# Optimization experiments

Measured on AMD Instinct MI355X. Metric: run time of the kernel, lower is better.

## Reference

```python
import jax, jax.numpy as jnp
import numpy as np

N_NODES = 50000
N_EDGES = 1_600_000
D_IN, D_HID, D_OUT = 128, 512, 64


def _graph_conv(h, src, dst, W_rel, b_rel, W_root, n_nodes):
    # PyG GraphConv with aggr='add':
    #   out_i = W_rel @ (sum_{j->i} h_j) + b_rel + W_root @ h_i
    agg = jax.ops.segment_sum(h[src], dst, num_segments=n_nodes)  # [N, d]
    return agg @ W_rel + b_rel + h @ W_root


def setup_inputs() -> dict:
    key = jax.random.key(0)
    ks = jax.random.split(key, 12)
    def glorot(k, shape):
        fan_in, fan_out = shape
        lim = (6.0 / (fan_in + fan_out)) ** 0.5
        return jax.random.uniform(k, shape, jnp.float32, -lim, lim)
    x = jax.random.normal(ks[0], (N_NODES, D_IN), jnp.float32)
    edge_index = jax.random.randint(ks[1], (2, N_EDGES), 0, N_NODES, jnp.int64)
    return {
        "x": x,
        "W1_rel": glorot(ks[2], (D_IN, D_HID)),
        "b1": jnp.zeros((D_HID,), jnp.float32),
        "W1_root": glorot(ks[3], (D_IN, D_HID)),
        "W2_rel": glorot(ks[4], (D_HID, D_HID)),
        "b2": jnp.zeros((D_HID,), jnp.float32),
        "W2_root": glorot(ks[5], (D_HID, D_HID)),
        "W3_rel": glorot(ks[6], (D_HID, D_HID)),
        "b3": jnp.zeros((D_HID,), jnp.float32),
        "W3_root": glorot(ks[7], (D_HID, D_HID)),
        "W_lin": glorot(ks[8], (D_HID, D_OUT)),
        "b_lin": jnp.zeros((D_OUT,), jnp.float32),
        "edge_index": edge_index,
    }


def reference(x, W1_rel, b1, W1_root, W2_rel, b2, W2_root,
              W3_rel, b3, W3_root, W_lin, b_lin, edge_index):
    n = x.shape[0]
    src, dst = edge_index[0], edge_index[1]
    h = jax.nn.relu(_graph_conv(x, src, dst, W1_rel, b1, W1_root, n))
    h = jax.nn.relu(_graph_conv(h, src, dst, W2_rel, b2, W2_root, n))
    h = jax.nn.relu(_graph_conv(h, src, dst, W3_rel, b3, W3_root, n))
    node_embed = h
    # dropout is identity in eval mode; final linear head
    logits = h @ W_lin + b_lin
    return (logits, node_embed)
```

## Files before the change

### kernel.cpp

```cpp
#include <hip/hip_runtime.h>


typedef unsigned short u16;
typedef unsigned int u32;
typedef unsigned char u8;

#define NN 50000
#define NE 1600000
#define MPAD 50176
#define GRID_M ((NN + 127) / 128)
#define NBKT 98
#define CAP 20480
#define STG 18432

using frag8 = __attribute__((ext_vector_type(8))) short;
using f32x4 = __attribute__((ext_vector_type(4))) float;
using f32x2 = __attribute__((ext_vector_type(2))) float;

__device__ __forceinline__ u16 f2bf(float f) {
  u32 u = __float_as_uint(f);
  u32 r = u + 0x7fffu + ((u >> 16) & 1u);
  return (u16)(r >> 16);
}
__device__ __forceinline__ float lo2f(u32 u) { return __uint_as_float(u << 16); }
__device__ __forceinline__ float hi2f(u32 u) { return __uint_as_float(u & 0xffff0000u); }
__device__ __forceinline__ u32 pack2(float a, float b) {
  return (u32)f2bf(a) | ((u32)f2bf(b) << 16);
}

__device__ __forceinline__ void g2l16(const void* g, void* l) {
  __builtin_amdgcn_global_load_lds((const __attribute__((address_space(1))) void*)g,
                                   (__attribute__((address_space(3))) void*)l, 16, 0, 0);
}

__device__ __forceinline__ int swz(int s) { return s ^ ((s >> 3) & 3); }


__global__ void zero_i32(int* p, int n) {
  int i = blockIdx.x * 256 + threadIdx.x;
  if (i < n) p[i] = 0;
}

__global__ __launch_bounds__(256) void p1bin(const int* __restrict__ src,
                                             const int* __restrict__ dst,
                                             int* __restrict__ gcur,
                                             u32* __restrict__ region, int ne) {
  __shared__ u32 lbuf[NBKT * 64];
  __shared__ int lcnt[NBKT];
  __shared__ int gbase[NBKT];
  const int tid = threadIdx.x;
  if (tid < NBKT) lcnt[tid] = 0;
  __syncthreads();
  const int base = blockIdx.x * 2048;
#pragma unroll
  for (int j = 0; j < 8; ++j) {
    int i = base + j * 256 + tid;
    if (i < ne) {
      int d = dst[i];
      int s = src[i];
      int b = d >> 9;
      u32 entry = ((u32)(d & 511) << 16) | (u32)s;
      int slot = atomicAdd(&lcnt[b], 1);
      if (slot < 64) lbuf[b * 64 + slot] = entry;
      else {
        int g = atomicAdd(&gcur[b], 1);
        region[(size_t)b * CAP + g] = entry;
      }
    }
  }
  __syncthreads();
  if (tid < NBKT) {
    int c = min(lcnt[tid], 64);
    gbase[tid] = atomicAdd(&gcur[tid], c);
  }
  __syncthreads();
  const int wv = tid >> 6, lane = tid & 63;
  for (int b = wv; b < NBKT; b += 4) {
    int c = min(lcnt[b], 64);
    int gb = gbase[b];
    for (int s2 = lane; s2 < c; s2 += 64)
      region[(size_t)b * CAP + gb + s2] = lbuf[b * 64 + s2];
  }
}

__global__ void scan98(const int* __restrict__ gcur, int* __restrict__ bbase,
                       int* __restrict__ rs) {
  if (threadIdx.x == 0) {
    int run = 0;
    for (int b = 0; b < NBKT; ++b) {
      bbase[b] = run;
      run += gcur[b];
    }
    bbase[NBKT] = run;
    rs[NN] = run;
  }
}

__global__ __launch_bounds__(256) void p2build(const u32* __restrict__ region,
                                               const int* __restrict__ gcnt,
                                               const int* __restrict__ bbase,
                                               int* __restrict__ rs,
                                               u16* __restrict__ csr) {
  __shared__ int cnt[512];
  __shared__ int off[512];
  __shared__ int sh[256];
  __shared__ u16 stg[STG];
  const int b = blockIdx.x, tid = threadIdx.x;
  const int n0 = b * 512;
  const int nnb = min(512, NN - n0);
  const int ec = gcnt[b];
  const int gb = bbase[b];
  const u32* __restrict__ reg = region + (size_t)b * CAP;
  cnt[tid] = 0;
  cnt[tid + 256] = 0;
  __syncthreads();
  for (int i = tid; i < ec; i += 256) atomicAdd(&cnt[reg[i] >> 16], 1);
  __syncthreads();
  int c0 = cnt[2 * tid], c1 = cnt[2 * tid + 1];
  int s = c0 + c1;
  sh[tid] = s;
  __syncthreads();
  for (int o = 1; o < 256; o <<= 1) {
    int t2 = (tid >= o) ? sh[tid - o] : 0;
    __syncthreads();
    sh[tid] += t2;
    __syncthreads();
  }
  int base0 = sh[tid] - s;
  off[2 * tid] = base0;
  off[2 * tid + 1] = base0 + c0;
  __syncthreads();
  if (2 * tid < nnb) rs[n0 + 2 * tid] = gb + off[2 * tid];
  if (2 * tid + 1 < nnb) rs[n0 + 2 * tid + 1] = gb + off[2 * tid + 1];
  cnt[2 * tid] = off[2 * tid];
  cnt[2 * tid + 1] = off[2 * tid + 1];
  __syncthreads();
  for (int i = tid; i < ec; i += 256) {
    u32 e = reg[i];
    int slot = atomicAdd(&cnt[e >> 16], 1);
    u16 sv = (u16)(e & 0xffff);
    if (slot < STG) stg[slot] = sv;
    else csr[gb + slot] = sv;
  }
  __syncthreads();
  for (int i = tid; i < ec && i < STG; i += 256) csr[gb + i] = stg[i];
}


__global__ void f2bf_x(const float4* __restrict__ in, u16* __restrict__ out, int n4) {
  int i = blockIdx.x * 256 + threadIdx.x;
  if (i < n4) {
    float4 v = in[i];
    int node = i >> 5;
    int w = i & 31;
    uint2 o;
    o.x = pack2(v.x, v.y);
    o.y = pack2(v.z, v.w);
    *(uint2*)(out + (size_t)node * 256 + 128 + w * 4) = o;
  }
}

__global__ void wtrans(const float* __restrict__ Wa, int Ka, const float* __restrict__ Wb,
                       int Kb, int N, u16* __restrict__ out) {
  int idx = blockIdx.x * 256 + threadIdx.x;
  int Kt = Ka + Kb;
  if (idx >= N * Kt) return;
  int n = idx / Kt;
  int k = idx - n * Kt;
  float v = (k < Ka) ? Wa[(size_t)k * N + n] : Wb[(size_t)(k - Ka) * N + n];
  out[idx] = f2bf(v);
}


__device__ __forceinline__ void accb(f32x2* a, uint4 v, float s) {
  f32x2 sv = (f32x2){s, s};
  f32x2 f;
  f.x = lo2f(v.x); f.y = hi2f(v.x); a[0] += f * sv;
  f.x = lo2f(v.y); f.y = hi2f(v.y); a[1] += f * sv;
  f.x = lo2f(v.z); f.y = hi2f(v.z); a[2] += f * sv;
  f.x = lo2f(v.w); f.y = hi2f(v.w); a[3] += f * sv;
}

__global__ __launch_bounds__(256) void agg_bf128(const u16* __restrict__ H, int ldh,
                                                 u16* __restrict__ Out, int ldo,
                                                 const int* __restrict__ rs,
                                                 const u16* __restrict__ csr, int n) {
  int w = (blockIdx.x * 256 + threadIdx.x) >> 6;
  int lane = threadIdx.x & 63;
  if (w >= n) return;
  int beg = rs[w], end = rs[w + 1];
  const int q = lane >> 4;
  const int lsub = lane & 15;
  f32x2 acc[4];
#pragma unroll
  for (int i = 0; i < 4; ++i) acc[i] = (f32x2){0.f, 0.f};

  int e = beg;
  for (; e + 16 <= end; e += 16) {
    int si[4];
#pragma unroll
    for (int u = 0; u < 4; ++u) si[u] = csr[e + 4 * u + q];
    uint4 v[4];
#pragma unroll
    for (int u = 0; u < 4; ++u)
      v[u] = *(const uint4*)(H + (size_t)si[u] * ldh + lsub * 8);
#pragma unroll
    for (int u = 0; u < 4; ++u) accb(acc, v[u], 1.f);
  }
  if (e < end) {
#pragma unroll
    for (int u = 0; u < 4; ++u) {
      int ei = e + 4 * u + q;
      int ec = min(ei, end - 1);
      int s0 = csr[ec];
      uint4 v = *(const uint4*)(H + (size_t)s0 * ldh + lsub * 8);
      accb(acc, v, (ei < end) ? 1.f : 0.f);
    }
  }
#pragma unroll
  for (int i = 0; i < 4; ++i) {
    acc[i].x += __shfl_xor(acc[i].x, 16);
    acc[i].y += __shfl_xor(acc[i].y, 16);
    acc[i].x += __shfl_xor(acc[i].x, 32);
    acc[i].y += __shfl_xor(acc[i].y, 32);
  }
  if (lane < 32) {
    int qq = lane >> 4;
    uint2 o;
    o.x = pack2(acc[qq * 2].x, acc[qq * 2].y);
    o.y = pack2(acc[qq * 2 + 1].x, acc[qq * 2 + 1].y);
    *(uint2*)(Out + (size_t)w * ldo + (lane & 15) * 8 + qq * 4) = o;
  }
}


__device__ __forceinline__ void accp(f32x2* a, uint4 v, float s) {
  f32x2 sv = (f32x2){s, s};
  f32x2 f;
  f = __builtin_amdgcn_cvt_pk_f32_fp8(v.x, false); a[0] += f * sv;
  f = __builtin_amdgcn_cvt_pk_f32_fp8(v.x, true);  a[1] += f * sv;
  f = __builtin_amdgcn_cvt_pk_f32_fp8(v.y, false); a[2] += f * sv;
  f = __builtin_amdgcn_cvt_pk_f32_fp8(v.y, true);  a[3] += f * sv;
  f = __builtin_amdgcn_cvt_pk_f32_fp8(v.z, false); a[4] += f * sv;
  f = __builtin_amdgcn_cvt_pk_f32_fp8(v.z, true);  a[5] += f * sv;
  f = __builtin_amdgcn_cvt_pk_f32_fp8(v.w, false); a[6] += f * sv;
  f = __builtin_amdgcn_cvt_pk_f32_fp8(v.w, true);  a[7] += f * sv;
}

__global__ __launch_bounds__(256) void agg_fp8(const u8* __restrict__ H8,
                                               const float* __restrict__ sc,
                                               u16* __restrict__ Out,
                                               const int* __restrict__ rs,
                                               const u16* __restrict__ csr, int n) {
  int w = (blockIdx.x * 256 + threadIdx.x) >> 6;
  int lane = threadIdx.x & 63;
  if (w >= n) return;
  int beg = rs[w], end = rs[w + 1];
  const int halfe = lane >> 5;
  const int lsub = lane & 31;
  const int shalf = lsub >> 4;
  f32x2 acc[8];
#pragma unroll
  for (int i = 0; i < 8; ++i) acc[i] = (f32x2){0.f, 0.f};

  int e = beg;
  for (; e + 8 <= end; e += 8) {
    int si[4];
#pragma unroll
    for (int u = 0; u < 4; ++u) si[u] = csr[e + 2 * u + halfe];
    uint4 v[4];
#pragma unroll
    for (int u = 0; u < 4; ++u)
      v[u] = *(const uint4*)(H8 + (size_t)si[u] * 512 + lsub * 16);
    float cs[4];
#pragma unroll
    for (int u = 0; u < 4; ++u) cs[u] = sc[si[u] * 2 + shalf];
#pragma unroll
    for (int u = 0; u < 4; ++u) accp(acc, v[u], cs[u]);
  }
  if (e < end) {
#pragma unroll
    for (int u = 0; u < 4; ++u) {
      int ei = e + 2 * u + halfe;
      int ec = min(ei, end - 1);
      int s0 = csr[ec];
      uint4 v = *(const uint4*)(H8 + (size_t)s0 * 512 + lsub * 16);
      float c = (ei < end) ? sc[s0 * 2 + shalf] : 0.f;
      accp(acc, v, c);
    }
  }
#pragma unroll
  for (int i = 0; i < 8; ++i) {
    acc[i].x += __shfl_xor(acc[i].x, 32);
    acc[i].y += __shfl_xor(acc[i].y, 32);
  }
  uint4 o;
  if (halfe == 0) {
    o.x = pack2(acc[0].x, acc[0].y);
    o.y = pack2(acc[1].x, acc[1].y);
    o.z = pack2(acc[2].x, acc[2].y);
    o.w = pack2(acc[3].x, acc[3].y);
  } else {
    o.x = pack2(acc[4].x, acc[4].y);
    o.y = pack2(acc[5].x, acc[5].y);
    o.z = pack2(acc[6].x, acc[6].y);
    o.w = pack2(acc[7].x, acc[7].y);
  }
  *(uint4*)(Out + (size_t)w * 512 + lsub * 16 + halfe * 8) = o;
}


__global__ __launch_bounds__(512, 4) void gemm256(
    const u16* __restrict__ A1, int lda1, const u16* __restrict__ A2, int lda2, int K1,
    int Ktot, const u16* __restrict__ Bt, const float* __restrict__ bias, int relu,
    u16* __restrict__ out_bf, int ldob, float* __restrict__ out_f32, int ldof,
    u8* __restrict__ out_fp8, float* __restrict__ out_sc, int M) {
  __shared__ u16 lA[3][128 * 32];
  __shared__ u16 lB[3][256 * 32];
  __shared__ u32 smaxu[128];
  const int tid = threadIdx.x;
  const int lane = tid & 63;
  const int wv = tid >> 6;
  const int wm = (wv >> 2) * 64;
  const int wn = (wv & 3) * 64;
  const int n0 = blockIdx.x * 256;
  const int m0 = blockIdx.y * 128;
  const int r15 = lane & 15;
  const int quad = lane >> 4;

  if (tid < 128) smaxu[tid] = 0;

  const int arow = tid >> 2;
  const int akc = ((tid & 3) ^ ((tid >> 3) & 3)) * 8;

  auto stage = [&](int kk, int b) {
    const u16* Ab;
    int lda;
    if (kk < K1) { Ab = A1 + kk; lda = lda1; }
    else         { Ab = A2 + (kk - K1); lda = lda2; }
    g2l16(Ab + (size_t)(m0 + arow) * lda + akc, &lA[b][tid * 8]);
#pragma unroll
    for (int i = 0; i < 2; ++i) {
      int li = tid + i * 512;
      int kc = ((li & 3) ^ ((li >> 3) & 3)) * 8;
      g2l16(Bt + (size_t)(n0 + (li >> 2)) * Ktot + (kk + kc), &lB[b][li * 8]);
    }
  };

  f32x4 acc[4][4];
#pragma unroll
  for (int i = 0; i < 4; ++i)
#pragma unroll
    for (int j = 0; j < 4; ++j) acc[i][j] = (f32x4){0.f, 0.f, 0.f, 0.f};

  const int ntk = Ktot >> 5;
  stage(0, 0);
  stage(32, 1);
  for (int t = 0; t < ntk; ++t) {
    const int cur = t % 3;
    __builtin_amdgcn_s_barrier();
    if (t + 2 < ntk) stage((t + 2) * 32, (t + 2) % 3);
    if (t + 2 < ntk)      asm volatile("s_waitcnt vmcnt(6)" ::: "memory");
    else if (t + 1 < ntk) asm volatile("s_waitcnt vmcnt(3)" ::: "memory");
    else                  asm volatile("s_waitcnt vmcnt(0)" ::: "memory");
    __builtin_amdgcn_s_barrier();
    __builtin_amdgcn_sched_barrier(0);
    frag8 af[4], bfr[4];
#pragma unroll
    for (int mt = 0; mt < 4; ++mt) {
      int s = (wm + mt * 16 + r15) * 4 + quad;
      af[mt] = *(const frag8*)&lA[cur][swz(s) * 8];
    }
#pragma unroll
    for (int nt = 0; nt < 4; ++nt) {
      int s = (wn + nt * 16 + r15) * 4 + quad;
      bfr[nt] = *(const frag8*)&lB[cur][swz(s) * 8];
    }
#pragma unroll
    for (int mt = 0; mt < 4; ++mt)
#pragma unroll
      for (int nt = 0; nt < 4; ++nt)
        acc[mt][nt] =
            __builtin_amdgcn_mfma_f32_16x16x32_bf16(af[mt], bfr[nt], acc[mt][nt], 0, 0, 0);
  }
  __syncthreads();

#pragma unroll
  for (int mt = 0; mt < 4; ++mt) {
#pragma unroll
    for (int r = 0; r < 4; ++r) {
      float rm = 0.f;
#pragma unroll
      for (int nt = 0; nt < 4; ++nt) {
        int c = n0 + wn + nt * 16 + r15;
        float v = acc[mt][nt][r] + bias[c];
        if (relu) v = fmaxf(v, 0.f);
        acc[mt][nt][r] = v;
        rm = fmaxf(rm, v);
      }
      if (out_fp8) {
        rm = fmaxf(rm, __shfl_xor(rm, 1));
        rm = fmaxf(rm, __shfl_xor(rm, 2));
        rm = fmaxf(rm, __shfl_xor(rm, 4));
        rm = fmaxf(rm, __shfl_xor(rm, 8));
        if (r15 == 0) atomicMax(&smaxu[wm + mt * 16 + quad * 4 + r], __float_as_uint(rm));
      }
    }
  }
  if (out_fp8) __syncthreads();

#pragma unroll
  for (int mt = 0; mt < 4; ++mt) {
    int rloc = wm + mt * 16 + quad * 4;
#pragma unroll
    for (int r = 0; r < 4; ++r) {
      int row = m0 + rloc + r;
      if (row < M) {
        float inv = 0.f;
        if (out_fp8) {
          float s = __uint_as_float(smaxu[rloc + r]);
          inv = (s > 0.f) ? 448.f / s : 0.f;
          if (r15 == 0 && wn == 0)
            out_sc[row * 2 + (n0 >> 8)] = (s > 0.f) ? s / 448.f : 0.f;
        }
#pragma unroll
        for (int nt = 0; nt < 4; ++nt) {
          int c = n0 + wn + nt * 16 + r15;
          float v = acc[mt][nt][r];
          if (out_f32) out_f32[(size_t)row * ldof + c] = v;
          if (out_bf) out_bf[(size_t)row * ldob + c] = f2bf(v);
        }
        if (out_fp8) {
          u32 u01 = (u32)__builtin_amdgcn_cvt_pk_fp8_f32(acc[mt][0][r] * inv,
                                                         acc[mt][1][r] * inv, 0, false);
          u32 u23 = (u32)__builtin_amdgcn_cvt_pk_fp8_f32(acc[mt][2][r] * inv,
                                                         acc[mt][3][r] * inv, 0, false);
          size_t rb = (size_t)row * 512 + n0 + wn + r15;
          out_fp8[rb] = (u8)(u01 & 0xff);
          out_fp8[rb + 16] = (u8)((u01 >> 8) & 0xff);
          out_fp8[rb + 32] = (u8)(u23 & 0xff);
          out_fp8[rb + 48] = (u8)((u23 >> 8) & 0xff);
        }
      }
    }
  }
}


__global__ __launch_bounds__(256) void gemm64(
    const u16* __restrict__ A1, int lda1, int Ktot, const u16* __restrict__ Bt,
    const float* __restrict__ bias, float* __restrict__ out_f32, int ldof, int M) {
  __shared__ u16 lA[3][128 * 32];
  __shared__ u16 lB[3][64 * 32];
  const int tid = threadIdx.x;
  const int lane = tid & 63;
  const int wv = tid >> 6;
  const int wm = (wv >> 1) * 64;
  const int wn = (wv & 1) * 32;
  const int m0 = blockIdx.x * 128;
  const int r15 = lane & 15;
  const int quad = lane >> 4;

  auto stage = [&](int kk, int b) {
#pragma unroll
    for (int i = 0; i < 2; ++i) {
      int li = tid + i * 256;
      int kc = ((li & 3) ^ ((li >> 3) & 3)) * 8;
      g2l16(A1 + (size_t)(m0 + (li >> 2)) * lda1 + kk + kc, &lA[b][li * 8]);
    }
    {
      int kc = ((tid & 3) ^ ((tid >> 3) & 3)) * 8;
      g2l16(Bt + (size_t)(tid >> 2) * Ktot + (kk + kc), &lB[b][tid * 8]);
    }
  };

  f32x4 acc[4][2];
#pragma unroll
  for (int i = 0; i < 4; ++i)
#pragma unroll
    for (int j = 0; j < 2; ++j) acc[i][j] = (f32x4){0.f, 0.f, 0.f, 0.f};

  const int ntk = Ktot >> 5;
  stage(0, 0);
  stage(32, 1);
  for (int t = 0; t < ntk; ++t) {
    const int cur = t % 3;
    __builtin_amdgcn_s_barrier();
    if (t + 2 < ntk) stage((t + 2) * 32, (t + 2) % 3);
    if (t + 2 < ntk)      asm volatile("s_waitcnt vmcnt(6)" ::: "memory");
    else if (t + 1 < ntk) asm volatile("s_waitcnt vmcnt(3)" ::: "memory");
    else                  asm volatile("s_waitcnt vmcnt(0)" ::: "memory");
    __builtin_amdgcn_s_barrier();
    __builtin_amdgcn_sched_barrier(0);
    frag8 af[4], bfr[2];
#pragma unroll
    for (int mt = 0; mt < 4; ++mt) {
      int s = (wm + mt * 16 + r15) * 4 + quad;
      af[mt] = *(const frag8*)&lA[cur][swz(s) * 8];
    }
#pragma unroll
    for (int nt = 0; nt < 2; ++nt) {
      int s = (wn + nt * 16 + r15) * 4 + quad;
      bfr[nt] = *(const frag8*)&lB[cur][swz(s) * 8];
    }
#pragma unroll
    for (int mt = 0; mt < 4; ++mt)
#pragma unroll
      for (int nt = 0; nt < 2; ++nt)
        acc[mt][nt] =
            __builtin_amdgcn_mfma_f32_16x16x32_bf16(af[mt], bfr[nt], acc[mt][nt], 0, 0, 0);
  }

#pragma unroll
  for (int mt = 0; mt < 4; ++mt) {
    int rbase = m0 + wm + mt * 16 + quad * 4;
#pragma unroll
    for (int r = 0; r < 4; ++r) {
      int row = rbase + r;
      if (row < M) {
#pragma unroll
        for (int nt = 0; nt < 2; ++nt) {
          int c = wn + nt * 16 + r15;
          out_f32[(size_t)row * ldof + c] = acc[mt][nt][r] + bias[c];
        }
      }
    }
  }
}


extern "C" void kernel_launch(void* const* d_in, const int* in_sizes, int n_in, void* d_out,
                              int out_size, void* d_ws, size_t ws_size, hipStream_t stream) {
  const float* x = (const float*)d_in[0];
  const float* W1r = (const float*)d_in[1];
  const float* b1 = (const float*)d_in[2];
  const float* W1o = (const float*)d_in[3];
  const float* W2r = (const float*)d_in[4];
  const float* b2 = (const float*)d_in[5];
  const float* W2o = (const float*)d_in[6];
  const float* W3r = (const float*)d_in[7];
  const float* b3 = (const float*)d_in[8];
  const float* W3o = (const float*)d_in[9];
  const float* Wl = (const float*)d_in[10];
  const float* bl = (const float*)d_in[11];
  const int* src = (const int*)d_in[12];
  const int* dst = src + NE;

  size_t off = 0;
  char* ws = (char*)d_ws;
  auto take = [&](size_t bytes) -> void* {
    void* p = ws + off;
    off = (off + bytes + 255) & ~(size_t)255;
    return p;
  };
  u16* h13 = (u16*)take((size_t)MPAD * 512 * 2);
  u16* h2 = (u16*)take((size_t)MPAD * 512 * 2);
  u16* aggB = (u16*)take((size_t)MPAD * 512 * 2);
  u16* aggx = aggB;
  u8* hfp8 = (u8*)take((size_t)MPAD * 512);
  float* scb = (float*)take((size_t)MPAD * 2 * 4);
  u16* wt1 = (u16*)take((size_t)512 * 256 * 2);
  u16* wt2 = (u16*)take((size_t)512 * 1024 * 2);
  u16* wt3 = (u16*)take((size_t)512 * 1024 * 2);
  u16* wtl = (u16*)take((size_t)64 * 512 * 2);
  u32* region = (u32*)take((size_t)NBKT * CAP * 4);
  int* gcur = (int*)take(128 * 4);
  int* bbase = (int*)take(128 * 4);
  int* rs = (int*)take((size_t)(NN + 1) * 4);
  u16* csr = (u16*)take((size_t)NE * 2);

  float* out_logits = (float*)d_out;
  float* out_embed = out_logits + (size_t)NN * 64;

  zero_i32<<<1, 128, 0, stream>>>(gcur, NBKT);
  p1bin<<<(NE + 2047) / 2048, 256, 0, stream>>>(src, dst, gcur, region, NE);
  scan98<<<1, 64, 0, stream>>>(gcur, bbase, rs);
  p2build<<<NBKT, 256, 0, stream>>>(region, gcur, bbase, rs, csr);

  f2bf_x<<<(NN * 32 + 255) / 256, 256, 0, stream>>>((const float4*)x, aggx, NN * 32);
  wtrans<<<(512 * 256 + 255) / 256, 256, 0, stream>>>(W1r, 128, W1o, 128, 512, wt1);
  wtrans<<<(512 * 1024 + 255) / 256, 256, 0, stream>>>(W2r, 512, W2o, 512, 512, wt2);
  wtrans<<<(512 * 1024 + 255) / 256, 256, 0, stream>>>(W3r, 512, W3o, 512, 512, wt3);
  wtrans<<<(64 * 512 + 255) / 256, 256, 0, stream>>>(Wl, 512, Wl, 0, 64, wtl);

  agg_bf128<<<(NN + 3) / 4, 256, 0, stream>>>(aggx + 128, 256, aggx, 256, rs, csr, NN);
  gemm256<<<dim3(2, GRID_M), 512, 0, stream>>>(aggx, 256, aggx, 256, 256, 256, wt1, b1, 1,
                                               h13, 512, (float*)nullptr, 0, hfp8, scb, NN);
  agg_fp8<<<(NN + 3) / 4, 256, 0, stream>>>(hfp8, scb, aggB, rs, csr, NN);
  gemm256<<<dim3(2, GRID_M), 512, 0, stream>>>(aggB, 512, h13, 512, 512, 1024, wt2, b2, 1,
                                               h2, 512, (float*)nullptr, 0, hfp8, scb, NN);
  agg_fp8<<<(NN + 3) / 4, 256, 0, stream>>>(hfp8, scb, aggB, rs, csr, NN);
  gemm256<<<dim3(2, GRID_M), 512, 0, stream>>>(aggB, 512, h2, 512, 512, 1024, wt3, b3, 1,
                                               h13, 512, out_embed, 512, (u8*)nullptr,
                                               (float*)nullptr, NN);
  gemm64<<<GRID_M, 256, 0, stream>>>(h13, 512, 512, wtl, bl, out_logits, 64, NN);
}
```

Before: 738.4 us.

## Compute root-term GEMM in FP8 from quantized activations in hybrid kernel

Adds a hybrid GEMM kernel that handles the root (self) term with FP8 MFMA on the already-quantized fp8 activations and fp8-quantized root weights, and keeps the aggregated term in bf16. Per-row and per-column scales are applied to the accumulator partway through the K loop. This removes the bf16 copies of the hidden activations in layers 2 and 3, halving root-term operand traffic and using the faster fp8 MFMA. In exchange the root path loses precision and the scale handling depends on rescaling at fixed K steps.

After: 1.754 ms. 2.38x slower.

```diff
diff --git a/kernel.cpp b/kernel.cpp
--- a/kernel.cpp
+++ b/kernel.cpp
@@ -4,6 +4,7 @@
 typedef unsigned short u16;
 typedef unsigned int u32;
 typedef unsigned char u8;
+typedef long i64;
 
 #define NN 50000
 #define NE 1600000
@@ -171,6 +172,34 @@
   out[idx] = f2bf(v);
 }
 
+__global__ __launch_bounds__(256) void wtransf8(const float* __restrict__ W, int N,
+                                                u8* __restrict__ out,
+                                                float* __restrict__ sB) {
+  int n = blockIdx.x * 4 + (threadIdx.x >> 6);
+  int lane = threadIdx.x & 63;
+  if (n >= N) return;
+  float v[8];
+  float m = 0.f;
+#pragma unroll
+  for (int j = 0; j < 8; ++j) {
+    float x = W[(size_t)(lane * 8 + j) * N + n];
+    v[j] = x;
+    m = fmaxf(m, fabsf(x));
+  }
+#pragma unroll
+  for (int o = 1; o < 64; o <<= 1) m = fmaxf(m, __shfl_xor(m, o));
+  float inv = (m > 0.f) ? 448.f / m : 0.f;
+  uint2 o2;
+  u32 lo0 = (u32)__builtin_amdgcn_cvt_pk_fp8_f32(v[0] * inv, v[1] * inv, 0, false);
+  u32 hi0 = (u32)__builtin_amdgcn_cvt_pk_fp8_f32(v[2] * inv, v[3] * inv, 0, false);
+  u32 lo1 = (u32)__builtin_amdgcn_cvt_pk_fp8_f32(v[4] * inv, v[5] * inv, 0, false);
+  u32 hi1 = (u32)__builtin_amdgcn_cvt_pk_fp8_f32(v[6] * inv, v[7] * inv, 0, false);
+  o2.x = (lo0 & 0xffffu) | (hi0 << 16);
+  o2.y = (lo1 & 0xffffu) | (hi1 << 16);
+  *(uint2*)(out + (size_t)n * 512 + lane * 8) = o2;
+  if (lane == 0) sB[n] = (m > 0.f) ? m / 448.f : 1.0f;
+}
+
 
 __device__ __forceinline__ void accb(f32x2* a, uint4 v, float s) {
   f32x2 sv = (f32x2){s, s};
@@ -311,8 +340,8 @@
 
 
 __global__ __launch_bounds__(512, 4) void gemm256(
-    const u16* __restrict__ A1, int lda1, const u16* __restrict__ A2, int lda2, int K1,
-    int Ktot, const u16* __restrict__ Bt, const float* __restrict__ bias, int relu,
+    const u16* __restrict__ A1, int lda1, int Ktot, const u16* __restrict__ Bt,
+    const float* __restrict__ bias, int relu,
     u16* __restrict__ out_bf, int ldob, float* __restrict__ out_f32, int ldof,
     u8* __restrict__ out_fp8, float* __restrict__ out_sc, int M) {
   __shared__ u16 lA[3][128 * 32];
@@ -334,11 +363,7 @@
   const int akc = ((tid & 3) ^ ((tid >> 3) & 3)) * 8;
 
   auto stage = [&](int kk, int b) {
-    const u16* Ab;
-    int lda;
-    if (kk < K1) { Ab = A1 + kk; lda = lda1; }
-    else         { Ab = A2 + (kk - K1); lda = lda2; }
-    g2l16(Ab + (size_t)(m0 + arow) * lda + akc, &lA[b][tid * 8]);
+    g2l16(A1 + (size_t)(m0 + arow) * lda1 + kk + akc, &lA[b][tid * 8]);
 #pragma unroll
     for (int i = 0; i < 2; ++i) {
       int li = tid + i * 512;
@@ -421,7 +446,202 @@
           float s = __uint_as_float(smaxu[rloc + r]);
           inv = (s > 0.f) ? 448.f / s : 0.f;
           if (r15 == 0 && wn == 0)
-            out_sc[row * 2 + (n0 >> 8)] = (s > 0.f) ? s / 448.f : 0.f;
+            out_sc[row * 2 + (n0 >> 8)] = (s > 0.f) ? s / 448.f : 1.0f;
+        }
+#pragma unroll
+        for (int nt = 0; nt < 4; ++nt) {
+          int c = n0 + wn + nt * 16 + r15;
+          float v = acc[mt][nt][r];
+          if (out_f32) out_f32[(size_t)row * ldof + c] = v;
+          if (out_bf) out_bf[(size_t)row * ldob + c] = f2bf(v);
+        }
+        if (out_fp8) {
+          u32 u01 = (u32)__builtin_amdgcn_cvt_pk_fp8_f32(acc[mt][0][r] * inv,
+                                                         acc[mt][1][r] * inv, 0, false);
+          u32 u23 = (u32)__builtin_amdgcn_cvt_pk_fp8_f32(acc[mt][2][r] * inv,
+                                                         acc[mt][3][r] * inv, 0, false);
+          size_t rb = (size_t)row * 512 + n0 + wn + r15;
+          out_fp8[rb] = (u8)(u01 & 0xff);
+          out_fp8[rb + 16] = (u8)((u01 >> 8) & 0xff);
+          out_fp8[rb + 32] = (u8)(u23 & 0xff);
+          out_fp8[rb + 48] = (u8)((u23 >> 8) & 0xff);
+        }
+      }
+    }
+  }
+}
+
+
+__global__ __launch_bounds__(512, 4) void gemmh(
+    const u16* __restrict__ A1, const u8* __restrict__ A2,
+    const float* __restrict__ sA2, const u16* __restrict__ Bt1,
+    const u8* __restrict__ Bt2, const float* __restrict__ sB,
+    const float* __restrict__ bias,
+    u16* __restrict__ out_bf, int ldob, float* __restrict__ out_f32, int ldof,
+    u8* __restrict__ out_fp8, float* __restrict__ out_sc, int M) {
+  __shared__ u8 lA[3][128 * 64];
+  __shared__ u8 lB[3][256 * 64];
+  __shared__ u32 smaxu[128];
+  const int tid = threadIdx.x;
+  const int lane = tid & 63;
+  const int wv = tid >> 6;
+  const int wm = (wv >> 2) * 64;
+  const int wn = (wv & 3) * 64;
+  const int n0 = blockIdx.x * 256;
+  const int m0 = blockIdx.y * 128;
+  const int r15 = lane & 15;
+  const int quad = lane >> 4;
+
+  if (tid < 128) smaxu[tid] = 0;
+
+  const int arow = tid >> 2;
+  const int achk = (tid & 3) ^ ((tid >> 3) & 3);
+
+  auto stage = [&](int ts, int b) {
+    if (ts < 8) {
+      int kk = ts * 64;
+      g2l16(A2 + (size_t)(m0 + arow) * 512 + kk + achk * 16, &lA[b][tid * 16]);
+#pragma unroll
+      for (int i = 0; i < 2; ++i) {
+        int li = tid + i * 512;
+        int chk = (li & 3) ^ ((li >> 3) & 3);
+        g2l16(Bt2 + (size_t)(n0 + (li >> 2)) * 512 + kk + chk * 16, &lB[b][li * 16]);
+      }
+    } else {
+      int kk = (ts - 8) * 32;
+      g2l16(A1 + (size_t)(m0 + arow) * 512 + kk + achk * 8, &lA[b][tid * 16]);
+#pragma unroll
+      for (int i = 0; i < 2; ++i) {
+        int li = tid + i * 512;
+        int chk = (li & 3) ^ ((li >> 3) & 3);
+        g2l16(Bt1 + (size_t)(n0 + (li >> 2)) * 512 + kk + chk * 8, &lB[b][li * 16]);
+      }
+    }
+  };
+
+  f32x4 acc[4][4];
+#pragma unroll
+  for (int i = 0; i < 4; ++i)
+#pragma unroll
+    for (int j = 0; j < 4; ++j) acc[i][j] = (f32x4){0.f, 0.f, 0.f, 0.f};
+
+  const int ntk = 24;
+  stage(0, 0);
+  stage(1, 1);
+  for (int t = 0; t < ntk; ++t) {
+    const int cur = t % 3;
+    __builtin_amdgcn_s_barrier();
+    if (t + 2 < ntk) stage(t + 2, (t + 2) % 3);
+    if (t + 2 < ntk)      asm volatile("s_waitcnt vmcnt(6)" ::: "memory");
+    else if (t + 1 < ntk) asm volatile("s_waitcnt vmcnt(3)" ::: "memory");
+    else                  asm volatile("s_waitcnt vmcnt(0)" ::: "memory");
+    __builtin_amdgcn_s_barrier();
+    __builtin_amdgcn_sched_barrier(0);
+    if (t == 4) {
+#pragma unroll
+      for (int mt = 0; mt < 4; ++mt)
+#pragma unroll
+        for (int r = 0; r < 4; ++r) {
+          int row = m0 + wm + mt * 16 + quad * 4 + r;
+          float ra = sA2[row * 2] / sA2[row * 2 + 1];
+#pragma unroll
+          for (int nt = 0; nt < 4; ++nt) acc[mt][nt][r] *= ra;
+        }
+    }
+    if (t == 8) {
+#pragma unroll
+      for (int mt = 0; mt < 4; ++mt)
+#pragma unroll
+        for (int r = 0; r < 4; ++r) {
+          int row = m0 + wm + mt * 16 + quad * 4 + r;
+          float s1 = sA2[row * 2 + 1];
+#pragma unroll
+          for (int nt = 0; nt < 4; ++nt) {
+            int c = n0 + wn + nt * 16 + r15;
+            acc[mt][nt][r] *= s1 * sB[c];
+          }
+        }
+    }
+    if (t < 8) {
+#pragma unroll
+      for (int ks = 0; ks < 2; ++ks) {
+        i64 af[4], bfr[4];
+#pragma unroll
+        for (int mt = 0; mt < 4; ++mt) {
+          int s = (wm + mt * 16 + r15) * 4 + ks * 2 + (quad >> 1);
+          af[mt] = *(const i64*)&lA[cur][swz(s) * 16 + (quad & 1) * 8];
+        }
+#pragma unroll
+        for (int nt = 0; nt < 4; ++nt) {
+          int s = (wn + nt * 16 + r15) * 4 + ks * 2 + (quad >> 1);
+          bfr[nt] = *(const i64*)&lB[cur][swz(s) * 16 + (quad & 1) * 8];
+        }
+#pragma unroll
+        for (int mt = 0; mt < 4; ++mt)
+#pragma unroll
+          for (int nt = 0; nt < 4; ++nt)
+            acc[mt][nt] = __builtin_amdgcn_mfma_f32_16x16x32_fp8_fp8(af[mt], bfr[nt],
+                                                                     acc[mt][nt], 0, 0, 0);
+      }
+    } else {
+      frag8 af[4], bfr[4];
+#pragma unroll
+      for (int mt = 0; mt < 4; ++mt) {
+        int s = (wm + mt * 16 + r15) * 4 + quad;
+        af[mt] = *(const frag8*)&lA[cur][swz(s) * 16];
+      }
+#pragma unroll
+      for (int nt = 0; nt < 4; ++nt) {
+        int s = (wn + nt * 16 + r15) * 4 + quad;
+        bfr[nt] = *(const frag8*)&lB[cur][swz(s) * 16];
+      }
+#pragma unroll
+      for (int mt = 0; mt < 4; ++mt)
+#pragma unroll
+        for (int nt = 0; nt < 4; ++nt)
+          acc[mt][nt] =
+              __builtin_amdgcn_mfma_f32_16x16x32_bf16(af[mt], bfr[nt], acc[mt][nt], 0, 0, 0);
+    }
+  }
+  __syncthreads();
+
+#pragma unroll
+  for (int mt = 0; mt < 4; ++mt) {
+#pragma unroll
+    for (int r = 0; r < 4; ++r) {
+      float rm = 0.f;
+#pragma unroll
+      for (int nt = 0; nt < 4; ++nt) {
+        int c = n0 + wn + nt * 16 + r15;
+        float v = acc[mt][nt][r] + bias[c];
+        v = fmaxf(v, 0.f);
+        acc[mt][nt][r] = v;
+        rm = fmaxf(rm, v);
+      }
+      if (out_fp8) {
+        rm = fmaxf(rm, __shfl_xor(rm, 1));
+        rm = fmaxf(rm, __shfl_xor(rm, 2));
+        rm = fmaxf(rm, __shfl_xor(rm, 4));
+        rm = fmaxf(rm, __shfl_xor(rm, 8));
+        if (r15 == 0) atomicMax(&smaxu[wm + mt * 16 + quad * 4 + r], __float_as_uint(rm));
+      }
+    }
+  }
+  if (out_fp8) __syncthreads();
+
+#pragma unroll
+  for (int mt = 0; mt < 4; ++mt) {
+    int rloc = wm + mt * 16 + quad * 4;
+#pragma unroll
+    for (int r = 0; r < 4; ++r) {
+      int row = m0 + rloc + r;
+      if (row < M) {
+        float inv = 0.f;
+        if (out_fp8) {
+          float s = __uint_as_float(smaxu[rloc + r]);
+          inv = (s > 0.f) ? 448.f / s : 0.f;
+          if (r15 == 0 && wn == 0)
+            out_sc[row * 2 + (n0 >> 8)] = (s > 0.f) ? s / 448.f : 1.0f;
         }
 #pragma unroll
         for (int nt = 0; nt < 4; ++nt) {
@@ -554,14 +774,20 @@
     return p;
   };
   u16* h13 = (u16*)take((size_t)MPAD * 512 * 2);
-  u16* h2 = (u16*)take((size_t)MPAD * 512 * 2);
+  u16* h2b = (u16*)take((size_t)MPAD * 512 * 2);
   u16* aggB = (u16*)take((size_t)MPAD * 512 * 2);
   u16* aggx = aggB;
-  u8* hfp8 = (u8*)take((size_t)MPAD * 512);
-  float* scb = (float*)take((size_t)MPAD * 2 * 4);
+  u8* hfp8a = (u8*)take((size_t)MPAD * 512);
+  float* scba = (float*)take((size_t)MPAD * 2 * 4);
+  u8* hfp8b = (u8*)h2b;
+  float* scbb = (float*)((char*)h2b + (size_t)MPAD * 512);
   u16* wt1 = (u16*)take((size_t)512 * 256 * 2);
-  u16* wt2 = (u16*)take((size_t)512 * 1024 * 2);
-  u16* wt3 = (u16*)take((size_t)512 * 1024 * 2);
+  u16* wt2 = (u16*)take((size_t)512 * 512 * 2);
+  u16* wt3 = (u16*)take((size_t)512 * 512 * 2);
+  u8* wtf2 = (u8*)take((size_t)512 * 512);
+  float* sB2 = (float*)take(512 * 4);
+  u8* wtf3 = (u8*)take((size_t)512 * 512);
+  float* sB3 = (float*)take(512 * 4);
   u16* wtl = (u16*)take((size_t)64 * 512 * 2);
   u32* region = (u32*)take((size_t)NBKT * CAP * 4);
   int* gcur = (int*)take(128 * 4);
@@ -579,19 +805,23 @@
 
   f2bf_x<<<(NN * 32 + 255) / 256, 256, 0, stream>>>((const float4*)x, aggx, NN * 32);
   wtrans<<<(512 * 256 + 255) / 256, 256, 0, stream>>>(W1r, 128, W1o, 128, 512, wt1);
-  wtrans<<<(512 * 1024 + 255) / 256, 256, 0, stream>>>(W2r, 512, W2o, 512, 512, wt2);
-  wtrans<<<(512 * 1024 + 255) / 256, 256, 0, stream>>>(W3r, 512, W3o, 512, 512, wt3);
+  wtrans<<<(512 * 512 + 255) / 256, 256, 0, stream>>>(W2r, 512, W2r, 0, 512, wt2);
+  wtrans<<<(512 * 512 + 255) / 256, 256, 0, stream>>>(W3r, 512, W3r, 0, 512, wt3);
+  wtransf8<<<128, 256, 0, stream>>>(W2o, 512, wtf2, sB2);
+  wtransf8<<<128, 256, 0, stream>>>(W3o, 512, wtf3, sB3);
   wtrans<<<(64 * 512 + 255) / 256, 256, 0, stream>>>(Wl, 512, Wl, 0, 64, wtl);
 
   agg_bf128<<<(NN + 3) / 4, 256, 0, stream>>>(aggx + 128, 256, aggx, 256, rs, csr, NN);
-  gemm256<<<dim3(2, GRID_M), 512, 0, stream>>>(aggx, 256, aggx, 256, 256, 256, wt1, b1, 1,
-                                               h13, 512, (float*)nullptr, 0, hfp8, scb, NN);
-  agg_fp8<<<(NN + 3) / 4, 256, 0, stream>>>(hfp8, scb, aggB, rs, csr, NN);
-  gemm256<<<dim3(2, GRID_M), 512, 0, stream>>>(aggB, 512, h13, 512, 512, 1024, wt2, b2, 1,
-                                               h2, 512, (float*)nullptr, 0, hfp8, scb, NN);
-  agg_fp8<<<(NN + 3) / 4, 256, 0, stream>>>(hfp8, scb, aggB, rs, csr, NN);
-  gemm256<<<dim3(2, GRID_M), 512, 0, stream>>>(aggB, 512, h2, 512, 512, 1024, wt3, b3, 1,
-                                               h13, 512, out_embed, 512, (u8*)nullptr,
-                                               (float*)nullptr, NN);
+  gemm256<<<dim3(2, GRID_M), 512, 0, stream>>>(aggx, 256, 256, wt1, b1, 1,
+                                               (u16*)nullptr, 0, (float*)nullptr, 0,
+                                               hfp8a, scba, NN);
+  agg_fp8<<<(NN + 3) / 4, 256, 0, stream>>>(hfp8a, scba, aggB, rs, csr, NN);
+  gemmh<<<dim3(2, GRID_M), 512, 0, stream>>>(aggB, hfp8a, scba, wt2, wtf2, sB2, b2,
+                                             (u16*)nullptr, 0, (float*)nullptr, 0,
+                                             hfp8b, scbb, NN);
+  agg_fp8<<<(NN + 3) / 4, 256, 0, stream>>>(hfp8b, scbb, aggB, rs, csr, NN);
+  gemmh<<<dim3(2, GRID_M), 512, 0, stream>>>(aggB, hfp8b, scbb, wt3, wtf3, sB3, b3,
+                                             h13, 512, out_embed, 512,
+                                             (u8*)nullptr, (float*)nullptr, NN);
   gemm64<<<GRID_M, 256, 0, stream>>>(h13, 512, 512, wtl, bl, out_logits, 64, NN);
 }
```
